# Kernel optimization log

Hardware: AMD Instinct MI355X
Metric: run time of the kernel (lower is better)

The kernel has to match this reference:

```python
import jax, jax.numpy as jnp
import numpy as np
from jax import lax

T, IMG, C_IN = 2048, 84, 4
HID = 256
NUM_OUT = 18
FEAT = 6 * 6 * 32  # 84 -> 42 -> 21 -> 11 -> 6 with stride-2 SAME convs


def setup_inputs() -> dict:
    key = jax.random.key(0)
    ks = jax.random.split(key, 8)
    d = {}
    d["x"] = jax.random.normal(ks[0], (T, IMG, IMG, C_IN), jnp.float32)
    cin = C_IN
    for i in range(4):
        d[f"conv_w{i}"] = jax.random.normal(ks[1 + i], (3, 3, cin, 32), jnp.float32) * (1.0 / np.sqrt(9 * cin))
        d[f"conv_b{i}"] = jnp.zeros((32,), jnp.float32)
        cin = 32
    d["lstm_w"] = jax.random.normal(ks[5], (FEAT + HID, 4 * HID), jnp.float32) * (1.0 / np.sqrt(FEAT + HID))
    d["lstm_b"] = jnp.zeros((4 * HID,), jnp.float32)
    d["fc_w"] = jax.random.normal(ks[6], (HID, NUM_OUT), jnp.float32) * 0.01
    d["fc_b"] = jnp.zeros((NUM_OUT,), jnp.float32)
    d["c_in"] = jnp.zeros((1, HID), jnp.float32)
    d["h_in"] = jnp.zeros((1, HID), jnp.float32)
    return d


def _conv_stack(x, ws, bs):
    dn = ("NHWC", "HWIO", "NHWC")
    for w, b in zip(ws, bs):
        x = jax.nn.elu(lax.conv_general_dilated(x, w, (2, 2), "SAME", dimension_numbers=dn) + b)
    return x.reshape(x.shape[0], -1)  # [T, FEAT]


def _lstm(feats, c0, h0, lstm_w, lstm_b):
    # BasicLSTMCell: gates [i, j, f, o], forget_bias = 1.0
    def step(carry, xt):
        c, h = carry  # [1, HID] each
        z = jnp.concatenate([xt[None, :], h], axis=1) @ lstm_w + lstm_b
        i, j, f, o = jnp.split(z, 4, axis=1)
        c = c * jax.nn.sigmoid(f + 1.0) + jax.nn.sigmoid(i) * jnp.tanh(j)
        h = jnp.tanh(c) * jax.nn.sigmoid(o)
        return (c, h), h[0]

    (_, _), hs = lax.scan(step, (c0, h0), feats)
    return hs  # [T, HID]


def reference(x, c_in, h_in,
              conv_w0, conv_b0, conv_w1, conv_b1,
              conv_w2, conv_b2, conv_w3, conv_b3,
              lstm_w, lstm_b, fc_w, fc_b):
    feats = _conv_stack(x, [conv_w0, conv_w1, conv_w2, conv_w3],
                        [conv_b0, conv_b1, conv_b2, conv_b3])
    hs = _lstm(feats, c_in, h_in, lstm_w, lstm_b)
    logits = hs @ fc_w + fc_b  # [T, NUM_OUT]
    return logits, hs
```

## Files before the change

kernel.cpp:

```cpp
#include <hip/hip_runtime.h>
#include <hip/hip_bf16.h>

__device__ inline float fsig(float x) { return 1.0f / (1.0f + __expf(-x)); }
__device__ inline float ftanh(float x) {
    float ax = fabsf(x);
    float e = __expf(-2.0f * ax);
    float r = (1.0f - e) / (1.0f + e);
    return x >= 0.0f ? r : -r;
}
__device__ inline float felu(float x) { return x > 0.0f ? x : expm1f(x); }

typedef _Float16 h2_t __attribute__((ext_vector_type(2)));

__device__ inline unsigned int packh2(float a, float b) {
    unsigned short ua = __builtin_bit_cast(unsigned short, (_Float16)a);
    unsigned short ub = __builtin_bit_cast(unsigned short, (_Float16)b);
    return (unsigned int)ua | ((unsigned int)ub << 16);
}
__device__ inline unsigned short f16bits(float a) {
    return __builtin_bit_cast(unsigned short, (_Float16)a);
}

__device__ inline float dot2acc(unsigned int w, unsigned int h, float acc) {
#if __has_builtin(__builtin_amdgcn_fdot2)
    return __builtin_amdgcn_fdot2(__builtin_bit_cast(h2_t, w), __builtin_bit_cast(h2_t, h), acc, false);
#else
    _Float16 wlo = __builtin_bit_cast(_Float16, (unsigned short)(w & 0xffff));
    _Float16 whi = __builtin_bit_cast(_Float16, (unsigned short)(w >> 16));
    _Float16 hlo = __builtin_bit_cast(_Float16, (unsigned short)(h & 0xffff));
    _Float16 hhi = __builtin_bit_cast(_Float16, (unsigned short)(h >> 16));
    return acc + (float)wlo * (float)hlo + (float)whi * (float)hhi;
#endif
}

__global__ __launch_bounds__(256) void conv0_kernel(const float* __restrict__ in,
                                                    const float* __restrict__ wg,
                                                    const float* __restrict__ bias,
                                                    unsigned short* __restrict__ out) {
    constexpr int W = 84, OW = 42, PAD = 0, WP = W + 2;
    __shared__ float in_s[3 * WP * 4];
    constexpr int NQ = 3 * WP;
    const int tid = threadIdx.x;
    const int oy = blockIdx.x;
    const int t = blockIdx.y;
    const int co = tid & 31;

    for (int q = tid; q < NQ; q += 256) {
        int ky = q / WP;
        int col = q - ky * WP;
        int iy = 2 * oy - PAD + ky;
        int ix = col - 1;
        float4 v = make_float4(0.f, 0.f, 0.f, 0.f);
        if (iy >= 0 && iy < W && ix >= 0 && ix < W)
            v = *(const float4*)&in[(((size_t)t * W + iy) * W + ix) * 4];
        *(float4*)&in_s[q * 4] = v;
    }

    float wr[9][4];
#pragma unroll
    for (int tap = 0; tap < 9; ++tap)
#pragma unroll
        for (int j = 0; j < 4; ++j) wr[tap][j] = wg[(tap * 4 + j) * 32 + co];
    __syncthreads();

    const int g = tid >> 5;
    constexpr int NOX = (OW + 7) / 8;
    float acc[NOX];
#pragma unroll
    for (int m = 0; m < NOX; ++m) acc[m] = 0.f;
#pragma unroll
    for (int ky = 0; ky < 3; ++ky)
#pragma unroll
        for (int kx = 0; kx < 3; ++kx) {
            float w0 = wr[ky * 3 + kx][0], w1 = wr[ky * 3 + kx][1];
            float w2 = wr[ky * 3 + kx][2], w3 = wr[ky * 3 + kx][3];
#pragma unroll
            for (int m = 0; m < NOX; ++m) {
                int ox = g + 8 * m;
                if (ox < OW) {
                    int cs = 2 * ox + kx - PAD + 1;
                    float4 xi = *(const float4*)&in_s[(ky * WP + cs) * 4];
                    acc[m] += xi.x * w0 + xi.y * w1 + xi.z * w2 + xi.w * w3;
                }
            }
        }
    float b = bias[co];
#pragma unroll
    for (int m = 0; m < NOX; ++m) {
        int ox = g + 8 * m;
        if (ox < OW)
            out[(((size_t)t * OW + oy) * OW + ox) * 32 + co] = f16bits(felu(acc[m] + b));
    }
}

template <int W, int OW, int PAD, bool F32OUT>
__global__ __launch_bounds__(256) void convh_kernel(const unsigned short* __restrict__ in,
                                                    const float* __restrict__ wg,
                                                    const float* __restrict__ bias,
                                                    void* __restrict__ outv) {
    constexpr int WP = W + 2;
    constexpr int OWH = (OW + 1) / 2;
    __shared__ __align__(16) unsigned short in_s[3][WP][32];
    __shared__ float zs[4][OW * 32];

    const int tid = threadIdx.x;
    const int oy = blockIdx.x;
    const int t = blockIdx.y;
    const int co = tid & 31;
    const int cig = (tid >> 5) & 3;
    const int oxh = tid >> 7;

    constexpr int NQ4 = 3 * WP * 4;
    uint4* in_s4 = reinterpret_cast<uint4*>(&in_s[0][0][0]);
    for (int q = tid; q < NQ4; q += 256) {
        int ky = q / (WP * 4);
        int rem = q - ky * (WP * 4);
        int col = rem >> 2, c4 = rem & 3;
        int iy = 2 * oy - PAD + ky;
        int ix = col - 1;
        uint4 v = make_uint4(0u, 0u, 0u, 0u);
        if (iy >= 0 && iy < W && ix >= 0 && ix < W)
            v = *(const uint4*)&in[(((size_t)t * W + iy) * W + ix) * 32 + c4 * 8];
        in_s4[q] = v;
    }

    unsigned int wr[9][4];
#pragma unroll
    for (int tap = 0; tap < 9; ++tap)
#pragma unroll
        for (int p = 0; p < 4; ++p)
            wr[tap][p] = packh2(wg[(tap * 32 + cig * 8 + 2 * p) * 32 + co],
                                wg[(tap * 32 + cig * 8 + 2 * p + 1) * 32 + co]);
    __syncthreads();

    float acc[OWH];
#pragma unroll
    for (int m = 0; m < OWH; ++m) acc[m] = 0.f;
#pragma unroll
    for (int ky = 0; ky < 3; ++ky)
#pragma unroll
        for (int kx = 0; kx < 3; ++kx) {
            unsigned int w0 = wr[ky * 3 + kx][0], w1 = wr[ky * 3 + kx][1];
            unsigned int w2 = wr[ky * 3 + kx][2], w3 = wr[ky * 3 + kx][3];
#pragma unroll
            for (int m = 0; m < OWH; ++m) {
                int ox = oxh * OWH + m;
                if (ox < OW) {
                    int cs = 2 * ox + kx - PAD + 1;
                    uint4 h8 = *(const uint4*)&in_s[ky][cs][cig * 8];
                    acc[m] = dot2acc(w0, h8.x, acc[m]);
                    acc[m] = dot2acc(w1, h8.y, acc[m]);
                    acc[m] = dot2acc(w2, h8.z, acc[m]);
                    acc[m] = dot2acc(w3, h8.w, acc[m]);
                }
            }
        }
#pragma unroll
    for (int m = 0; m < OWH; ++m) {
        int ox = oxh * OWH + m;
        if (ox < OW) zs[cig][ox * 32 + co] = acc[m];
    }
    __syncthreads();

    for (int idx = tid; idx < OW * 32; idx += 256) {
        float s = zs[0][idx] + zs[1][idx] + zs[2][idx] + zs[3][idx] + bias[idx & 31];
        s = felu(s);
        if constexpr (F32OUT)
            ((float*)outv)[(((size_t)t * OW + oy) * OW) * 32 + idx] = s;
        else
            ((unsigned short*)outv)[(((size_t)t * OW + oy) * OW) * 32 + idx] = f16bits(s);
    }
}

__global__ void gemm_kernel(const float* __restrict__ A, const float* __restrict__ Wx,
                            const float* __restrict__ bias, float* __restrict__ C) {
    __shared__ float As[32][64];
    __shared__ float Bs[32][64];
    const int bn = blockIdx.x, bm = blockIdx.y;
    const int tx = threadIdx.x, ty = threadIdx.y;
    const int tid = ty * 16 + tx;
    float acc[4][4] = {};
    for (int k0 = 0; k0 < 1152; k0 += 32) {
        {
            int r = tid >> 3;
            int c = (tid & 7) * 4;
            float4 a0 = *(const float4*)&A[(size_t)(bm * 64 + r) * 1152 + k0 + c];
            float4 a1 = *(const float4*)&A[(size_t)(bm * 64 + r + 32) * 1152 + k0 + c];
            As[c + 0][r] = a0.x; As[c + 1][r] = a0.y; As[c + 2][r] = a0.z; As[c + 3][r] = a0.w;
            As[c + 0][r + 32] = a1.x; As[c + 1][r + 32] = a1.y; As[c + 2][r + 32] = a1.z; As[c + 3][r + 32] = a1.w;
            int rb = tid >> 4;
            int cb = (tid & 15) * 4;
            *(float4*)&Bs[rb][cb] = *(const float4*)&Wx[(size_t)(k0 + rb) * 1024 + bn * 64 + cb];
            *(float4*)&Bs[rb + 16][cb] = *(const float4*)&Wx[(size_t)(k0 + rb + 16) * 1024 + bn * 64 + cb];
        }
        __syncthreads();
#pragma unroll
        for (int kk = 0; kk < 32; ++kk) {
            float4 a = *(float4*)&As[kk][ty * 4];
            float4 b = *(float4*)&Bs[kk][tx * 4];
            acc[0][0] += a.x * b.x; acc[0][1] += a.x * b.y; acc[0][2] += a.x * b.z; acc[0][3] += a.x * b.w;
            acc[1][0] += a.y * b.x; acc[1][1] += a.y * b.y; acc[1][2] += a.y * b.z; acc[1][3] += a.y * b.w;
            acc[2][0] += a.z * b.x; acc[2][1] += a.z * b.y; acc[2][2] += a.z * b.z; acc[2][3] += a.z * b.w;
            acc[3][0] += a.w * b.x; acc[3][1] += a.w * b.y; acc[3][2] += a.w * b.z; acc[3][3] += a.w * b.w;
        }
        __syncthreads();
    }
#pragma unroll
    for (int i = 0; i < 4; ++i) {
        int row = bm * 64 + ty * 4 + i;
#pragma unroll
        for (int j = 0; j < 4; ++j) {
            int col = bn * 64 + tx * 4 + j;
            C[(size_t)row * 1024 + col] = acc[i][j] + bias[col];
        }
    }
}

__global__ __launch_bounds__(512) void lstm9_kernel(const float* __restrict__ lstm_w,
                                                    const float* __restrict__ xpart,
                                                    const float* __restrict__ c_in,
                                                    const float* __restrict__ h_in,
                                                    float* __restrict__ hs_out) {
    __shared__ __align__(16) unsigned int wl[512][52];
    __shared__ __align__(16) unsigned short hpk[2][256];

    const int tid = threadIdx.x;
    const int wv = tid >> 6;
    const int l = tid & 63;
    const int s = l >> 5;
    const int u0 = (wv << 5) + (l & 31);

    for (int q = 0; q < 4; ++q)
        for (int p = 0; p < 12; ++p)
            wl[tid][q * 12 + p] = packh2(
                lstm_w[(size_t)(1152 + 128 * s + 2 * p) * 1024 + (q << 8) + u0],
                lstm_w[(size_t)(1152 + 128 * s + 2 * p + 1) * 1024 + (q << 8) + u0]);
    unsigned int wreg[4][52];
#pragma unroll
    for (int q = 0; q < 4; ++q)
        for (int p = 12; p < 64; ++p)
            wreg[q][p - 12] = packh2(
                lstm_w[(size_t)(1152 + 128 * s + 2 * p) * 1024 + (q << 8) + u0],
                lstm_w[(size_t)(1152 + 128 * s + 2 * p + 1) * 1024 + (q << 8) + u0]);

    float c_state = c_in[u0];
    if (tid < 256) hpk[0][tid] = f16bits(h_in[tid]);
    __syncthreads();

    float xp0 = xpart[u0], xp1 = xpart[256 + u0], xp2 = xpart[512 + u0], xp3 = xpart[768 + u0];

    for (int t = 0; t < 2048; ++t) {
        const int cur = t & 1;
        const uint4* hq = reinterpret_cast<const uint4*>(&hpk[cur][s << 7]);

        float a0 = 0.f, a1 = 0.f, a2 = 0.f, a3 = 0.f;
        {
            uint4 hA = hq[0], hB = hq[1], hC = hq[2];
            uint4 w0a = *(const uint4*)&wl[tid][0];
            uint4 w0b = *(const uint4*)&wl[tid][4];
            uint4 w0c = *(const uint4*)&wl[tid][8];
            a0 = dot2acc(w0a.x, hA.x, a0); a0 = dot2acc(w0a.y, hA.y, a0);
            a0 = dot2acc(w0a.z, hA.z, a0); a0 = dot2acc(w0a.w, hA.w, a0);
            a0 = dot2acc(w0b.x, hB.x, a0); a0 = dot2acc(w0b.y, hB.y, a0);
            a0 = dot2acc(w0b.z, hB.z, a0); a0 = dot2acc(w0b.w, hB.w, a0);
            a0 = dot2acc(w0c.x, hC.x, a0); a0 = dot2acc(w0c.y, hC.y, a0);
            a0 = dot2acc(w0c.z, hC.z, a0); a0 = dot2acc(w0c.w, hC.w, a0);
            uint4 w1a = *(const uint4*)&wl[tid][12];
            uint4 w1b = *(const uint4*)&wl[tid][16];
            uint4 w1c = *(const uint4*)&wl[tid][20];
            a1 = dot2acc(w1a.x, hA.x, a1); a1 = dot2acc(w1a.y, hA.y, a1);
            a1 = dot2acc(w1a.z, hA.z, a1); a1 = dot2acc(w1a.w, hA.w, a1);
            a1 = dot2acc(w1b.x, hB.x, a1); a1 = dot2acc(w1b.y, hB.y, a1);
            a1 = dot2acc(w1b.z, hB.z, a1); a1 = dot2acc(w1b.w, hB.w, a1);
            a1 = dot2acc(w1c.x, hC.x, a1); a1 = dot2acc(w1c.y, hC.y, a1);
            a1 = dot2acc(w1c.z, hC.z, a1); a1 = dot2acc(w1c.w, hC.w, a1);
            uint4 w2a = *(const uint4*)&wl[tid][24];
            uint4 w2b = *(const uint4*)&wl[tid][28];
            uint4 w2c = *(const uint4*)&wl[tid][32];
            a2 = dot2acc(w2a.x, hA.x, a2); a2 = dot2acc(w2a.y, hA.y, a2);
            a2 = dot2acc(w2a.z, hA.z, a2); a2 = dot2acc(w2a.w, hA.w, a2);
            a2 = dot2acc(w2b.x, hB.x, a2); a2 = dot2acc(w2b.y, hB.y, a2);
            a2 = dot2acc(w2b.z, hB.z, a2); a2 = dot2acc(w2b.w, hB.w, a2);
            a2 = dot2acc(w2c.x, hC.x, a2); a2 = dot2acc(w2c.y, hC.y, a2);
            a2 = dot2acc(w2c.z, hC.z, a2); a2 = dot2acc(w2c.w, hC.w, a2);
            uint4 w3a = *(const uint4*)&wl[tid][36];
            uint4 w3b = *(const uint4*)&wl[tid][40];
            uint4 w3c = *(const uint4*)&wl[tid][44];
            a3 = dot2acc(w3a.x, hA.x, a3); a3 = dot2acc(w3a.y, hA.y, a3);
            a3 = dot2acc(w3a.z, hA.z, a3); a3 = dot2acc(w3a.w, hA.w, a3);
            a3 = dot2acc(w3b.x, hB.x, a3); a3 = dot2acc(w3b.y, hB.y, a3);
            a3 = dot2acc(w3b.z, hB.z, a3); a3 = dot2acc(w3b.w, hB.w, a3);
            a3 = dot2acc(w3c.x, hC.x, a3); a3 = dot2acc(w3c.y, hC.y, a3);
            a3 = dot2acc(w3c.z, hC.z, a3); a3 = dot2acc(w3c.w, hC.w, a3);
        }
#pragma unroll
        for (int c = 3; c < 16; ++c) {
            uint4 h4 = hq[c];
            const int r = 4 * (c - 3);
            a0 = dot2acc(wreg[0][r + 0], h4.x, a0); a0 = dot2acc(wreg[0][r + 1], h4.y, a0);
            a0 = dot2acc(wreg[0][r + 2], h4.z, a0); a0 = dot2acc(wreg[0][r + 3], h4.w, a0);
            a1 = dot2acc(wreg[1][r + 0], h4.x, a1); a1 = dot2acc(wreg[1][r + 1], h4.y, a1);
            a1 = dot2acc(wreg[1][r + 2], h4.z, a1); a1 = dot2acc(wreg[1][r + 3], h4.w, a1);
            a2 = dot2acc(wreg[2][r + 0], h4.x, a2); a2 = dot2acc(wreg[2][r + 1], h4.y, a2);
            a2 = dot2acc(wreg[2][r + 2], h4.z, a2); a2 = dot2acc(wreg[2][r + 3], h4.w, a2);
            a3 = dot2acc(wreg[3][r + 0], h4.x, a3); a3 = dot2acc(wreg[3][r + 1], h4.y, a3);
            a3 = dot2acc(wreg[3][r + 2], h4.z, a3); a3 = dot2acc(wreg[3][r + 3], h4.w, a3);
        }

        float xn0 = 0.f, xn1 = 0.f, xn2 = 0.f, xn3 = 0.f;
        if (t + 1 < 2048) {
            const float* xr = &xpart[(size_t)(t + 1) * 1024];
            xn0 = xr[u0]; xn1 = xr[256 + u0]; xn2 = xr[512 + u0]; xn3 = xr[768 + u0];
        }

        float zi = a0 + __shfl_xor(a0, 32, 64) + xp0;
        float zj = a1 + __shfl_xor(a1, 32, 64) + xp1;
        float zf = a2 + __shfl_xor(a2, 32, 64) + xp2;
        float zo = a3 + __shfl_xor(a3, 32, 64) + xp3;

        c_state = c_state * fsig(zf + 1.0f) + fsig(zi) * ftanh(zj);
        float h = ftanh(c_state) * fsig(zo);
        if (s == 0) {
            hs_out[(size_t)t * 256 + u0] = h;
            hpk[cur ^ 1][u0] = f16bits(h);
        }

        asm volatile("s_waitcnt lgkmcnt(0)\n\ts_barrier" ::: "memory");
        xp0 = xn0; xp1 = xn1; xp2 = xn2; xp3 = xn3;
    }
}

__global__ void logits_kernel(const float* __restrict__ hs, const float* __restrict__ fc_w,
                              const float* __restrict__ fc_b, float* __restrict__ out) {
    int idx = blockIdx.x * 256 + threadIdx.x;
    if (idx >= 2048 * 18) return;
    int t = idx / 18, n = idx % 18;
    float acc = fc_b[n];
    const float* hrow = hs + (size_t)t * 256;
#pragma unroll 4
    for (int k = 0; k < 256; ++k) acc += hrow[k] * fc_w[k * 18 + n];
    out[idx] = acc;
}

extern "C" void kernel_launch(void* const* d_in, const int* in_sizes, int n_in,
                              void* d_out, int out_size, void* d_ws, size_t ws_size,
                              hipStream_t stream) {
    const float* x   = (const float*)d_in[0];
    const float* w0  = (const float*)d_in[1];
    const float* b0  = (const float*)d_in[2];
    const float* w1  = (const float*)d_in[3];
    const float* b1  = (const float*)d_in[4];
    const float* w2  = (const float*)d_in[5];
    const float* b2  = (const float*)d_in[6];
    const float* w3  = (const float*)d_in[7];
    const float* b3  = (const float*)d_in[8];
    const float* lw  = (const float*)d_in[9];
    const float* lb  = (const float*)d_in[10];
    const float* fcw = (const float*)d_in[11];
    const float* fcb = (const float*)d_in[12];
    const float* cin = (const float*)d_in[13];
    const float* hin = (const float*)d_in[14];

    float* outp = (float*)d_out;
    float* hs_out = outp + 2048 * 18;

    const size_t FIXED_B = ((size_t)2048 * 1152 + (size_t)2048 * 1024) * 4;
    const size_t PERT_B = ((size_t)56448 + 14112 + 3872) * 2;

    int C = 128;
    const int cands[5] = {2048, 1024, 512, 256, 128};
    for (int i = 0; i < 5; ++i) {
        if (FIXED_B + (size_t)cands[i] * PERT_B <= ws_size) { C = cands[i]; break; }
    }

    float* feats = (float*)d_ws;
    float* xpart = feats + (size_t)2048 * 1152;
    unsigned short* c0buf = (unsigned short*)(xpart + (size_t)2048 * 1024);
    unsigned short* c1buf = c0buf + (size_t)C * 56448;
    unsigned short* c2buf = c1buf + (size_t)C * 14112;

    for (int t0 = 0; t0 < 2048; t0 += C) {
        const float* xin = x + (size_t)t0 * 84 * 84 * 4;
        conv0_kernel<<<dim3(42, C), 256, 0, stream>>>(xin, w0, b0, c0buf);
        convh_kernel<42, 21, 0, false><<<dim3(21, C), 256, 0, stream>>>(c0buf, w1, b1, c1buf);
        convh_kernel<21, 11, 1, false><<<dim3(11, C), 256, 0, stream>>>(c1buf, w2, b2, c2buf);
        convh_kernel<11, 6, 1, true><<<dim3(6, C), 256, 0, stream>>>(c2buf, w3, b3,
                                                                     feats + (size_t)t0 * 1152);
    }

    gemm_kernel<<<dim3(16, 32), dim3(16, 16), 0, stream>>>(feats, lw, lb, xpart);
    lstm9_kernel<<<1, 512, 0, stream>>>(lw, xpart, cin, hin, hs_out);
    logits_kernel<<<144, 256, 0, stream>>>(hs_out, fcw, fcb, outp);
}
```

Baseline: 4.337 ms.

## Fuse conv stack, GEMM and LSTM into one persistent kernel with overlapped chunks

All conv layers, the input-projection GEMM and the LSTM recurrence now run in one persistent launch of 256 blocks. Block 0 runs the sequential LSTM and waits on per-chunk counters. The other 255 blocks work through 128-timestep chunks of conv layers and GEMM, separated by global atomic barriers. This lets the LSTM scan start on early chunks while later chunks are still being convolved, hiding the conv front end behind the serial recurrence. The cost is spin-wait barriers, which need every block to be resident at once (deadlock risk otherwise), a fixed chunk size, and a different LSTM reduction layout.

```diff
diff --git a/kernel.cpp b/kernel.cpp
--- a/kernel.cpp
+++ b/kernel.cpp
@@ -1,5 +1,8 @@
 #include <hip/hip_runtime.h>
 #include <hip/hip_bf16.h>
+
+#define AGENT __HIP_MEMORY_SCOPE_AGENT
+#define NW 255
 
 __device__ inline float fsig(float x) { return 1.0f / (1.0f + __expf(-x)); }
 __device__ inline float ftanh(float x) {
@@ -33,29 +36,47 @@
 #endif
 }
 
-__global__ __launch_bounds__(256) void conv0_kernel(const float* __restrict__ in,
-                                                    const float* __restrict__ wg,
-                                                    const float* __restrict__ bias,
-                                                    unsigned short* __restrict__ out) {
-    constexpr int W = 84, OW = 42, PAD = 0, WP = W + 2;
-    __shared__ float in_s[3 * WP * 4];
-    constexpr int NQ = 3 * WP;
+__global__ void init_kernel(unsigned int* ctrs) {
+    int i = threadIdx.x;
+    if (i < 80) ctrs[i] = 0u;
+}
+
+__device__ inline void layer_barrier(unsigned int* ctr) {
+    __syncthreads();
+    if (threadIdx.x == 0) {
+        __threadfence();
+        __hip_atomic_fetch_add(ctr, 1u, __ATOMIC_RELEASE, AGENT);
+        while (__hip_atomic_load(ctr, __ATOMIC_ACQUIRE, AGENT) < (unsigned)NW)
+            __builtin_amdgcn_s_sleep(2);
+    }
+    __syncthreads();
+}
+
+__device__ inline void lstm_wait_chunk(unsigned int* ctrs, int c) {
+    if (threadIdx.x == 0) {
+        unsigned int* f = ctrs + c * 5 + 4;
+        while (__hip_atomic_load(f, __ATOMIC_ACQUIRE, AGENT) < (unsigned)NW)
+            __builtin_amdgcn_s_sleep(2);
+    }
+    __syncthreads();
+}
+
+__device__ void conv0_item(const float* __restrict__ x, const float* __restrict__ wg,
+                           const float* __restrict__ bias, unsigned short* __restrict__ out,
+                           int tg, int tl, int oy, unsigned char* smraw) {
+    constexpr int W = 84, OW = 42, WP = 86;
+    float* in_s = (float*)smraw;
     const int tid = threadIdx.x;
-    const int oy = blockIdx.x;
-    const int t = blockIdx.y;
     const int co = tid & 31;
 
-    for (int q = tid; q < NQ; q += 256) {
-        int ky = q / WP;
-        int col = q - ky * WP;
-        int iy = 2 * oy - PAD + ky;
-        int ix = col - 1;
+    for (int q = tid; q < 3 * WP; q += 512) {
+        int ky = q / WP, col = q - ky * WP;
+        int iy = 2 * oy + ky, ix = col - 1;
         float4 v = make_float4(0.f, 0.f, 0.f, 0.f);
-        if (iy >= 0 && iy < W && ix >= 0 && ix < W)
-            v = *(const float4*)&in[(((size_t)t * W + iy) * W + ix) * 4];
+        if (iy < W && ix >= 0 && ix < W)
+            v = *(const float4*)&x[(((size_t)tg * W + iy) * W + ix) * 4];
         *(float4*)&in_s[q * 4] = v;
     }
-
     float wr[9][4];
 #pragma unroll
     for (int tap = 0; tap < 9; ++tap)
@@ -64,10 +85,7 @@
     __syncthreads();
 
     const int g = tid >> 5;
-    constexpr int NOX = (OW + 7) / 8;
-    float acc[NOX];
-#pragma unroll
-    for (int m = 0; m < NOX; ++m) acc[m] = 0.f;
+    float acc[3] = {0.f, 0.f, 0.f};
 #pragma unroll
     for (int ky = 0; ky < 3; ++ky)
 #pragma unroll
@@ -75,10 +93,10 @@
             float w0 = wr[ky * 3 + kx][0], w1 = wr[ky * 3 + kx][1];
             float w2 = wr[ky * 3 + kx][2], w3 = wr[ky * 3 + kx][3];
 #pragma unroll
-            for (int m = 0; m < NOX; ++m) {
-                int ox = g + 8 * m;
+            for (int m = 0; m < 3; ++m) {
+                int ox = g + 16 * m;
                 if (ox < OW) {
-                    int cs = 2 * ox + kx - PAD + 1;
+                    int cs = 2 * ox + kx + 1;
                     float4 xi = *(const float4*)&in_s[(ky * WP + cs) * 4];
                     acc[m] += xi.x * w0 + xi.y * w1 + xi.z * w2 + xi.w * w3;
                 }
@@ -86,44 +104,39 @@
         }
     float b = bias[co];
 #pragma unroll
-    for (int m = 0; m < NOX; ++m) {
-        int ox = g + 8 * m;
+    for (int m = 0; m < 3; ++m) {
+        int ox = g + 16 * m;
         if (ox < OW)
-            out[(((size_t)t * OW + oy) * OW + ox) * 32 + co] = f16bits(felu(acc[m] + b));
-    }
+            out[(((size_t)tl * OW + oy) * OW + ox) * 32 + co] = f16bits(felu(acc[m] + b));
+    }
+    __syncthreads();
 }
 
 template <int W, int OW, int PAD, bool F32OUT>
-__global__ __launch_bounds__(256) void convh_kernel(const unsigned short* __restrict__ in,
-                                                    const float* __restrict__ wg,
-                                                    const float* __restrict__ bias,
-                                                    void* __restrict__ outv) {
+__device__ void convh_item(const unsigned short* __restrict__ in, const float* __restrict__ wg,
+                           const float* __restrict__ bias, void* __restrict__ outv,
+                           int tl_in, int oy, size_t orow, unsigned char* smraw) {
     constexpr int WP = W + 2;
-    constexpr int OWH = (OW + 1) / 2;
-    __shared__ __align__(16) unsigned short in_s[3][WP][32];
-    __shared__ float zs[4][OW * 32];
-
+    constexpr int OWQ = (OW + 3) / 4;
+    unsigned short* in_s = (unsigned short*)smraw;
+    float* zs = (float*)(smraw + 8448);
     const int tid = threadIdx.x;
-    const int oy = blockIdx.x;
-    const int t = blockIdx.y;
     const int co = tid & 31;
     const int cig = (tid >> 5) & 3;
-    const int oxh = tid >> 7;
-
-    constexpr int NQ4 = 3 * WP * 4;
-    uint4* in_s4 = reinterpret_cast<uint4*>(&in_s[0][0][0]);
-    for (int q = tid; q < NQ4; q += 256) {
+    const int oxq = tid >> 7;
+
+    const int NQ4 = 3 * WP * 4;
+    uint4* in_s4 = (uint4*)in_s;
+    for (int q = tid; q < NQ4; q += 512) {
         int ky = q / (WP * 4);
-        int rem = q - ky * (WP * 4);
+        int rem = q - ky * WP * 4;
         int col = rem >> 2, c4 = rem & 3;
-        int iy = 2 * oy - PAD + ky;
-        int ix = col - 1;
+        int iy = 2 * oy - PAD + ky, ix = col - 1;
         uint4 v = make_uint4(0u, 0u, 0u, 0u);
         if (iy >= 0 && iy < W && ix >= 0 && ix < W)
-            v = *(const uint4*)&in[(((size_t)t * W + iy) * W + ix) * 32 + c4 * 8];
+            v = *(const uint4*)&in[(((size_t)tl_in * W + iy) * W + ix) * 32 + c4 * 8];
         in_s4[q] = v;
     }
-
     unsigned int wr[9][4];
 #pragma unroll
     for (int tap = 0; tap < 9; ++tap)
@@ -133,9 +146,9 @@
                                 wg[(tap * 32 + cig * 8 + 2 * p + 1) * 32 + co]);
     __syncthreads();
 
-    float acc[OWH];
-#pragma unroll
-    for (int m = 0; m < OWH; ++m) acc[m] = 0.f;
+    float acc[OWQ];
+#pragma unroll
+    for (int m = 0; m < OWQ; ++m) acc[m] = 0.f;
 #pragma unroll
     for (int ky = 0; ky < 3; ++ky)
 #pragma unroll
@@ -143,11 +156,11 @@
             unsigned int w0 = wr[ky * 3 + kx][0], w1 = wr[ky * 3 + kx][1];
             unsigned int w2 = wr[ky * 3 + kx][2], w3 = wr[ky * 3 + kx][3];
 #pragma unroll
-            for (int m = 0; m < OWH; ++m) {
-                int ox = oxh * OWH + m;
+            for (int m = 0; m < OWQ; ++m) {
+                int ox = oxq * OWQ + m;
                 if (ox < OW) {
                     int cs = 2 * ox + kx - PAD + 1;
-                    uint4 h8 = *(const uint4*)&in_s[ky][cs][cig * 8];
+                    uint4 h8 = *(const uint4*)&in_s[(ky * WP + cs) * 32 + cig * 8];
                     acc[m] = dot2acc(w0, h8.x, acc[m]);
                     acc[m] = dot2acc(w1, h8.y, acc[m]);
                     acc[m] = dot2acc(w2, h8.z, acc[m]);
@@ -156,177 +169,234 @@
             }
         }
 #pragma unroll
-    for (int m = 0; m < OWH; ++m) {
-        int ox = oxh * OWH + m;
-        if (ox < OW) zs[cig][ox * 32 + co] = acc[m];
-    }
-    __syncthreads();
-
-    for (int idx = tid; idx < OW * 32; idx += 256) {
-        float s = zs[0][idx] + zs[1][idx] + zs[2][idx] + zs[3][idx] + bias[idx & 31];
+    for (int m = 0; m < OWQ; ++m) {
+        int ox = oxq * OWQ + m;
+        if (ox < OW) zs[cig * OW * 32 + ox * 32 + co] = acc[m];
+    }
+    __syncthreads();
+
+    for (int idx = tid; idx < OW * 32; idx += 512) {
+        float s = zs[idx] + zs[OW * 32 + idx] + zs[2 * OW * 32 + idx] + zs[3 * OW * 32 + idx] +
+                  bias[idx & 31];
         s = felu(s);
         if constexpr (F32OUT)
-            ((float*)outv)[(((size_t)t * OW + oy) * OW) * 32 + idx] = s;
+            ((float*)outv)[((orow * OW + oy) * OW) * 32 + idx] = s;
         else
-            ((unsigned short*)outv)[(((size_t)t * OW + oy) * OW) * 32 + idx] = f16bits(s);
-    }
-}
-
-__global__ void gemm_kernel(const float* __restrict__ A, const float* __restrict__ Wx,
-                            const float* __restrict__ bias, float* __restrict__ C) {
-    __shared__ float As[32][64];
-    __shared__ float Bs[32][64];
-    const int bn = blockIdx.x, bm = blockIdx.y;
-    const int tx = threadIdx.x, ty = threadIdx.y;
-    const int tid = ty * 16 + tx;
+            ((unsigned short*)outv)[((orow * OW + oy) * OW) * 32 + idx] = f16bits(s);
+    }
+    __syncthreads();
+}
+
+__device__ void gemm_item(const float* __restrict__ A, const float* __restrict__ Wx,
+                          const float* __restrict__ bias, float* __restrict__ C,
+                          int bm, int bn, unsigned char* smraw) {
+    float* As = (float*)smraw;
+    float* Bs = (float*)(smraw + 8192);
+    const int tid = threadIdx.x;
+    const bool act = tid < 256;
+    const int tx = tid & 15, ty = (tid >> 4) & 15;
     float acc[4][4] = {};
     for (int k0 = 0; k0 < 1152; k0 += 32) {
-        {
+        if (act) {
             int r = tid >> 3;
             int c = (tid & 7) * 4;
             float4 a0 = *(const float4*)&A[(size_t)(bm * 64 + r) * 1152 + k0 + c];
             float4 a1 = *(const float4*)&A[(size_t)(bm * 64 + r + 32) * 1152 + k0 + c];
-            As[c + 0][r] = a0.x; As[c + 1][r] = a0.y; As[c + 2][r] = a0.z; As[c + 3][r] = a0.w;
-            As[c + 0][r + 32] = a1.x; As[c + 1][r + 32] = a1.y; As[c + 2][r + 32] = a1.z; As[c + 3][r + 32] = a1.w;
+            As[(c + 0) * 64 + r] = a0.x; As[(c + 1) * 64 + r] = a0.y;
+            As[(c + 2) * 64 + r] = a0.z; As[(c + 3) * 64 + r] = a0.w;
+            As[(c + 0) * 64 + r + 32] = a1.x; As[(c + 1) * 64 + r + 32] = a1.y;
+            As[(c + 2) * 64 + r + 32] = a1.z; As[(c + 3) * 64 + r + 32] = a1.w;
             int rb = tid >> 4;
             int cb = (tid & 15) * 4;
-            *(float4*)&Bs[rb][cb] = *(const float4*)&Wx[(size_t)(k0 + rb) * 1024 + bn * 64 + cb];
-            *(float4*)&Bs[rb + 16][cb] = *(const float4*)&Wx[(size_t)(k0 + rb + 16) * 1024 + bn * 64 + cb];
+            *(float4*)&Bs[rb * 64 + cb] = *(const float4*)&Wx[(size_t)(k0 + rb) * 1024 + bn * 64 + cb];
+            *(float4*)&Bs[(rb + 16) * 64 + cb] =
+                *(const float4*)&Wx[(size_t)(k0 + rb + 16) * 1024 + bn * 64 + cb];
         }
         __syncthreads();
-#pragma unroll
-        for (int kk = 0; kk < 32; ++kk) {
-            float4 a = *(float4*)&As[kk][ty * 4];
-            float4 b = *(float4*)&Bs[kk][tx * 4];
-            acc[0][0] += a.x * b.x; acc[0][1] += a.x * b.y; acc[0][2] += a.x * b.z; acc[0][3] += a.x * b.w;
-            acc[1][0] += a.y * b.x; acc[1][1] += a.y * b.y; acc[1][2] += a.y * b.z; acc[1][3] += a.y * b.w;
-            acc[2][0] += a.z * b.x; acc[2][1] += a.z * b.y; acc[2][2] += a.z * b.z; acc[2][3] += a.z * b.w;
-            acc[3][0] += a.w * b.x; acc[3][1] += a.w * b.y; acc[3][2] += a.w * b.z; acc[3][3] += a.w * b.w;
+        if (act) {
+#pragma unroll
+            for (int kk = 0; kk < 32; ++kk) {
+                float4 a = *(float4*)&As[kk * 64 + ty * 4];
+                float4 b = *(float4*)&Bs[kk * 64 + tx * 4];
+                acc[0][0] += a.x * b.x; acc[0][1] += a.x * b.y; acc[0][2] += a.x * b.z; acc[0][3] += a.x * b.w;
+                acc[1][0] += a.y * b.x; acc[1][1] += a.y * b.y; acc[1][2] += a.y * b.z; acc[1][3] += a.y * b.w;
+                acc[2][0] += a.z * b.x; acc[2][1] += a.z * b.y; acc[2][2] += a.z * b.z; acc[2][3] += a.z * b.w;
+                acc[3][0] += a.w * b.x; acc[3][1] += a.w * b.y; acc[3][2] += a.w * b.z; acc[3][3] += a.w * b.w;
+            }
         }
         __syncthreads();
     }
-#pragma unroll
-    for (int i = 0; i < 4; ++i) {
-        int row = bm * 64 + ty * 4 + i;
-#pragma unroll
-        for (int j = 0; j < 4; ++j) {
-            int col = bn * 64 + tx * 4 + j;
-            C[(size_t)row * 1024 + col] = acc[i][j] + bias[col];
-        }
-    }
-}
-
-__global__ __launch_bounds__(512) void lstm9_kernel(const float* __restrict__ lstm_w,
-                                                    const float* __restrict__ xpart,
-                                                    const float* __restrict__ c_in,
-                                                    const float* __restrict__ h_in,
-                                                    float* __restrict__ hs_out) {
-    __shared__ __align__(16) unsigned int wl[512][52];
-    __shared__ __align__(16) unsigned short hpk[2][256];
-
+    if (act) {
+#pragma unroll
+        for (int i = 0; i < 4; ++i) {
+            int row = bm * 64 + ty * 4 + i;
+#pragma unroll
+            for (int j = 0; j < 4; ++j) {
+                int col = bn * 64 + tx * 4 + j;
+                C[(size_t)row * 1024 + col] = acc[i][j] + bias[col];
+            }
+        }
+    }
+    __syncthreads();
+}
+
+__global__ __launch_bounds__(512) void mega_kernel(
+    const float* __restrict__ x, const float* __restrict__ w0, const float* __restrict__ b0,
+    const float* __restrict__ w1, const float* __restrict__ b1,
+    const float* __restrict__ w2, const float* __restrict__ b2,
+    const float* __restrict__ w3, const float* __restrict__ b3,
+    const float* __restrict__ lw, const float* __restrict__ lb,
+    const float* __restrict__ cin, const float* __restrict__ hin,
+    unsigned short* c0buf, unsigned short* c1buf, unsigned short* c2buf,
+    float* feats, float* xpart, unsigned int* ctrs, float* hs_out) {
+    __shared__ __align__(16) unsigned char smraw[115776];
+    const int bid = blockIdx.x;
     const int tid = threadIdx.x;
-    const int wv = tid >> 6;
-    const int l = tid & 63;
-    const int s = l >> 5;
-    const int u0 = (wv << 5) + (l & 31);
-
-    for (int q = 0; q < 4; ++q)
-        for (int p = 0; p < 12; ++p)
-            wl[tid][q * 12 + p] = packh2(
-                lstm_w[(size_t)(1152 + 128 * s + 2 * p) * 1024 + (q << 8) + u0],
-                lstm_w[(size_t)(1152 + 128 * s + 2 * p + 1) * 1024 + (q << 8) + u0]);
-    unsigned int wreg[4][52];
-#pragma unroll
-    for (int q = 0; q < 4; ++q)
-        for (int p = 12; p < 64; ++p)
-            wreg[q][p - 12] = packh2(
-                lstm_w[(size_t)(1152 + 128 * s + 2 * p) * 1024 + (q << 8) + u0],
-                lstm_w[(size_t)(1152 + 128 * s + 2 * p + 1) * 1024 + (q << 8) + u0]);
-
-    float c_state = c_in[u0];
-    if (tid < 256) hpk[0][tid] = f16bits(h_in[tid]);
-    __syncthreads();
-
-    float xp0 = xpart[u0], xp1 = xpart[256 + u0], xp2 = xpart[512 + u0], xp3 = xpart[768 + u0];
-
-    for (int t = 0; t < 2048; ++t) {
-        const int cur = t & 1;
-        const uint4* hq = reinterpret_cast<const uint4*>(&hpk[cur][s << 7]);
-
-        float a0 = 0.f, a1 = 0.f, a2 = 0.f, a3 = 0.f;
-        {
-            uint4 hA = hq[0], hB = hq[1], hC = hq[2];
-            uint4 w0a = *(const uint4*)&wl[tid][0];
-            uint4 w0b = *(const uint4*)&wl[tid][4];
-            uint4 w0c = *(const uint4*)&wl[tid][8];
-            a0 = dot2acc(w0a.x, hA.x, a0); a0 = dot2acc(w0a.y, hA.y, a0);
-            a0 = dot2acc(w0a.z, hA.z, a0); a0 = dot2acc(w0a.w, hA.w, a0);
-            a0 = dot2acc(w0b.x, hB.x, a0); a0 = dot2acc(w0b.y, hB.y, a0);
-            a0 = dot2acc(w0b.z, hB.z, a0); a0 = dot2acc(w0b.w, hB.w, a0);
-            a0 = dot2acc(w0c.x, hC.x, a0); a0 = dot2acc(w0c.y, hC.y, a0);
-            a0 = dot2acc(w0c.z, hC.z, a0); a0 = dot2acc(w0c.w, hC.w, a0);
-            uint4 w1a = *(const uint4*)&wl[tid][12];
-            uint4 w1b = *(const uint4*)&wl[tid][16];
-            uint4 w1c = *(const uint4*)&wl[tid][20];
-            a1 = dot2acc(w1a.x, hA.x, a1); a1 = dot2acc(w1a.y, hA.y, a1);
-            a1 = dot2acc(w1a.z, hA.z, a1); a1 = dot2acc(w1a.w, hA.w, a1);
-            a1 = dot2acc(w1b.x, hB.x, a1); a1 = dot2acc(w1b.y, hB.y, a1);
-            a1 = dot2acc(w1b.z, hB.z, a1); a1 = dot2acc(w1b.w, hB.w, a1);
-            a1 = dot2acc(w1c.x, hC.x, a1); a1 = dot2acc(w1c.y, hC.y, a1);
-            a1 = dot2acc(w1c.z, hC.z, a1); a1 = dot2acc(w1c.w, hC.w, a1);
-            uint4 w2a = *(const uint4*)&wl[tid][24];
-            uint4 w2b = *(const uint4*)&wl[tid][28];
-            uint4 w2c = *(const uint4*)&wl[tid][32];
-            a2 = dot2acc(w2a.x, hA.x, a2); a2 = dot2acc(w2a.y, hA.y, a2);
-            a2 = dot2acc(w2a.z, hA.z, a2); a2 = dot2acc(w2a.w, hA.w, a2);
-            a2 = dot2acc(w2b.x, hB.x, a2); a2 = dot2acc(w2b.y, hB.y, a2);
-            a2 = dot2acc(w2b.z, hB.z, a2); a2 = dot2acc(w2b.w, hB.w, a2);
-            a2 = dot2acc(w2c.x, hC.x, a2); a2 = dot2acc(w2c.y, hC.y, a2);
-            a2 = dot2acc(w2c.z, hC.z, a2); a2 = dot2acc(w2c.w, hC.w, a2);
-            uint4 w3a = *(const uint4*)&wl[tid][36];
-            uint4 w3b = *(const uint4*)&wl[tid][40];
-            uint4 w3c = *(const uint4*)&wl[tid][44];
-            a3 = dot2acc(w3a.x, hA.x, a3); a3 = dot2acc(w3a.y, hA.y, a3);
-            a3 = dot2acc(w3a.z, hA.z, a3); a3 = dot2acc(w3a.w, hA.w, a3);
-            a3 = dot2acc(w3b.x, hB.x, a3); a3 = dot2acc(w3b.y, hB.y, a3);
-            a3 = dot2acc(w3b.z, hB.z, a3); a3 = dot2acc(w3b.w, hB.w, a3);
-            a3 = dot2acc(w3c.x, hC.x, a3); a3 = dot2acc(w3c.y, hC.y, a3);
-            a3 = dot2acc(w3c.z, hC.z, a3); a3 = dot2acc(w3c.w, hC.w, a3);
-        }
-#pragma unroll
-        for (int c = 3; c < 16; ++c) {
-            uint4 h4 = hq[c];
-            const int r = 4 * (c - 3);
-            a0 = dot2acc(wreg[0][r + 0], h4.x, a0); a0 = dot2acc(wreg[0][r + 1], h4.y, a0);
-            a0 = dot2acc(wreg[0][r + 2], h4.z, a0); a0 = dot2acc(wreg[0][r + 3], h4.w, a0);
-            a1 = dot2acc(wreg[1][r + 0], h4.x, a1); a1 = dot2acc(wreg[1][r + 1], h4.y, a1);
-            a1 = dot2acc(wreg[1][r + 2], h4.z, a1); a1 = dot2acc(wreg[1][r + 3], h4.w, a1);
-            a2 = dot2acc(wreg[2][r + 0], h4.x, a2); a2 = dot2acc(wreg[2][r + 1], h4.y, a2);
-            a2 = dot2acc(wreg[2][r + 2], h4.z, a2); a2 = dot2acc(wreg[2][r + 3], h4.w, a2);
-            a3 = dot2acc(wreg[3][r + 0], h4.x, a3); a3 = dot2acc(wreg[3][r + 1], h4.y, a3);
-            a3 = dot2acc(wreg[3][r + 2], h4.z, a3); a3 = dot2acc(wreg[3][r + 3], h4.w, a3);
-        }
-
-        float xn0 = 0.f, xn1 = 0.f, xn2 = 0.f, xn3 = 0.f;
-        if (t + 1 < 2048) {
-            const float* xr = &xpart[(size_t)(t + 1) * 1024];
-            xn0 = xr[u0]; xn1 = xr[256 + u0]; xn2 = xr[512 + u0]; xn3 = xr[768 + u0];
-        }
-
-        float zi = a0 + __shfl_xor(a0, 32, 64) + xp0;
-        float zj = a1 + __shfl_xor(a1, 32, 64) + xp1;
-        float zf = a2 + __shfl_xor(a2, 32, 64) + xp2;
-        float zo = a3 + __shfl_xor(a3, 32, 64) + xp3;
-
-        c_state = c_state * fsig(zf + 1.0f) + fsig(zi) * ftanh(zj);
-        float h = ftanh(c_state) * fsig(zo);
-        if (s == 0) {
-            hs_out[(size_t)t * 256 + u0] = h;
-            hpk[cur ^ 1][u0] = f16bits(h);
-        }
-
-        asm volatile("s_waitcnt lgkmcnt(0)\n\ts_barrier" ::: "memory");
-        xp0 = xn0; xp1 = xn1; xp2 = xn2; xp3 = xn3;
+
+    if (bid == 0) {
+        unsigned int (*wl)[52] = reinterpret_cast<unsigned int(*)[52]>(smraw);
+        float (*zsm)[4][256] = reinterpret_cast<float(*)[4][256]>(smraw + 106496);
+        unsigned int (*hpk)[2][68] = reinterpret_cast<unsigned int(*)[2][68]>(smraw + 114688);
+
+        const int s = tid >> 8;
+        const int u = tid & 255;
+
+        for (int q = 0; q < 4; ++q)
+            for (int p = 0; p < 12; ++p) {
+                int gp = 64 * s + p;
+                wl[tid][q * 12 + p] = packh2(
+                    lw[(size_t)(1152 + 2 * gp) * 1024 + (q << 8) + u],
+                    lw[(size_t)(1152 + 2 * gp + 1) * 1024 + (q << 8) + u]);
+            }
+        unsigned int wreg[4][52];
+#pragma unroll
+        for (int q = 0; q < 4; ++q)
+            for (int p = 12; p < 64; ++p) {
+                int gp = 64 * s + p;
+                wreg[q][p - 12] = packh2(
+                    lw[(size_t)(1152 + 2 * gp) * 1024 + (q << 8) + u],
+                    lw[(size_t)(1152 + 2 * gp + 1) * 1024 + (q << 8) + u]);
+            }
+
+        float c_state = cin[u];
+        if (tid < 256) {
+            unsigned short* hrow = (unsigned short*)&hpk[0][u >> 7][0];
+            hrow[u & 127] = f16bits(hin[u]);
+        }
+        __syncthreads();
+
+        lstm_wait_chunk(ctrs, 0);
+        float xp0 = xpart[u], xp1 = xpart[256 + u], xp2 = xpart[512 + u], xp3 = xpart[768 + u];
+
+        for (int t = 0; t < 2048; ++t) {
+            const int cur = t & 1;
+            const uint4* hq = reinterpret_cast<const uint4*>(&hpk[cur][s][0]);
+
+            float a0 = 0.f, a1 = 0.f, a2 = 0.f, a3 = 0.f;
+            {
+                uint4 hA = hq[0], hB = hq[1], hC = hq[2];
+                uint4 w0a = *(const uint4*)&wl[tid][0];
+                uint4 w0b = *(const uint4*)&wl[tid][4];
+                uint4 w0c = *(const uint4*)&wl[tid][8];
+                a0 = dot2acc(w0a.x, hA.x, a0); a0 = dot2acc(w0a.y, hA.y, a0);
+                a0 = dot2acc(w0a.z, hA.z, a0); a0 = dot2acc(w0a.w, hA.w, a0);
+                a0 = dot2acc(w0b.x, hB.x, a0); a0 = dot2acc(w0b.y, hB.y, a0);
+                a0 = dot2acc(w0b.z, hB.z, a0); a0 = dot2acc(w0b.w, hB.w, a0);
+                a0 = dot2acc(w0c.x, hC.x, a0); a0 = dot2acc(w0c.y, hC.y, a0);
+                a0 = dot2acc(w0c.z, hC.z, a0); a0 = dot2acc(w0c.w, hC.w, a0);
+                uint4 w1a = *(const uint4*)&wl[tid][12];
+                uint4 w1b = *(const uint4*)&wl[tid][16];
+                uint4 w1c = *(const uint4*)&wl[tid][20];
+                a1 = dot2acc(w1a.x, hA.x, a1); a1 = dot2acc(w1a.y, hA.y, a1);
+                a1 = dot2acc(w1a.z, hA.z, a1); a1 = dot2acc(w1a.w, hA.w, a1);
+                a1 = dot2acc(w1b.x, hB.x, a1); a1 = dot2acc(w1b.y, hB.y, a1);
+                a1 = dot2acc(w1b.z, hB.z, a1); a1 = dot2acc(w1b.w, hB.w, a1);
+                a1 = dot2acc(w1c.x, hC.x, a1); a1 = dot2acc(w1c.y, hC.y, a1);
+                a1 = dot2acc(w1c.z, hC.z, a1); a1 = dot2acc(w1c.w, hC.w, a1);
+                uint4 w2a = *(const uint4*)&wl[tid][24];
+                uint4 w2b = *(const uint4*)&wl[tid][28];
+                uint4 w2c = *(const uint4*)&wl[tid][32];
+                a2 = dot2acc(w2a.x, hA.x, a2); a2 = dot2acc(w2a.y, hA.y, a2);
+                a2 = dot2acc(w2a.z, hA.z, a2); a2 = dot2acc(w2a.w, hA.w, a2);
+                a2 = dot2acc(w2b.x, hB.x, a2); a2 = dot2acc(w2b.y, hB.y, a2);
+                a2 = dot2acc(w2b.z, hB.z, a2); a2 = dot2acc(w2b.w, hB.w, a2);
+                a2 = dot2acc(w2c.x, hC.x, a2); a2 = dot2acc(w2c.y, hC.y, a2);
+                a2 = dot2acc(w2c.z, hC.z, a2); a2 = dot2acc(w2c.w, hC.w, a2);
+                uint4 w3a = *(const uint4*)&wl[tid][36];
+                uint4 w3b = *(const uint4*)&wl[tid][40];
+                uint4 w3c = *(const uint4*)&wl[tid][44];
+                a3 = dot2acc(w3a.x, hA.x, a3); a3 = dot2acc(w3a.y, hA.y, a3);
+                a3 = dot2acc(w3a.z, hA.z, a3); a3 = dot2acc(w3a.w, hA.w, a3);
+                a3 = dot2acc(w3b.x, hB.x, a3); a3 = dot2acc(w3b.y, hB.y, a3);
+                a3 = dot2acc(w3b.z, hB.z, a3); a3 = dot2acc(w3b.w, hB.w, a3);
+                a3 = dot2acc(w3c.x, hC.x, a3); a3 = dot2acc(w3c.y, hC.y, a3);
+                a3 = dot2acc(w3c.z, hC.z, a3); a3 = dot2acc(w3c.w, hC.w, a3);
+            }
+#pragma unroll
+            for (int c = 3; c < 16; ++c) {
+                uint4 h4 = hq[c];
+                const int r = 4 * (c - 3);
+                a0 = dot2acc(wreg[0][r + 0], h4.x, a0); a0 = dot2acc(wreg[0][r + 1], h4.y, a0);
+                a0 = dot2acc(wreg[0][r + 2], h4.z, a0); a0 = dot2acc(wreg[0][r + 3], h4.w, a0);
+                a1 = dot2acc(wreg[1][r + 0], h4.x, a1); a1 = dot2acc(wreg[1][r + 1], h4.y, a1);
+                a1 = dot2acc(wreg[1][r + 2], h4.z, a1); a1 = dot2acc(wreg[1][r + 3], h4.w, a1);
+                a2 = dot2acc(wreg[2][r + 0], h4.x, a2); a2 = dot2acc(wreg[2][r + 1], h4.y, a2);
+                a2 = dot2acc(wreg[2][r + 2], h4.z, a2); a2 = dot2acc(wreg[2][r + 3], h4.w, a2);
+                a3 = dot2acc(wreg[3][r + 0], h4.x, a3); a3 = dot2acc(wreg[3][r + 1], h4.y, a3);
+                a3 = dot2acc(wreg[3][r + 2], h4.z, a3); a3 = dot2acc(wreg[3][r + 3], h4.w, a3);
+            }
+            zsm[s][0][u] = a0;
+            zsm[s][1][u] = a1;
+            zsm[s][2][u] = a2;
+            zsm[s][3][u] = a3;
+
+            float xn0 = 0.f, xn1 = 0.f, xn2 = 0.f, xn3 = 0.f;
+            if (t + 1 < 2048) {
+                if (((t + 1) & 127) == 0) lstm_wait_chunk(ctrs, (t + 1) >> 7);
+                const float* xr = &xpart[(size_t)(t + 1) * 1024];
+                xn0 = xr[u]; xn1 = xr[256 + u]; xn2 = xr[512 + u]; xn3 = xr[768 + u];
+            }
+
+            asm volatile("s_waitcnt lgkmcnt(0)\n\ts_barrier" ::: "memory");
+
+            float zi = zsm[0][0][u] + zsm[1][0][u] + xp0;
+            float zj = zsm[0][1][u] + zsm[1][1][u] + xp1;
+            float zf = zsm[0][2][u] + zsm[1][2][u] + xp2;
+            float zo = zsm[0][3][u] + zsm[1][3][u] + xp3;
+            c_state = c_state * fsig(zf + 1.0f) + fsig(zi) * ftanh(zj);
+            float h = ftanh(c_state) * fsig(zo);
+            if (tid < 256) {
+                hs_out[(size_t)t * 256 + u] = h;
+                unsigned short* hrow = (unsigned short*)&hpk[cur ^ 1][u >> 7][0];
+                hrow[u & 127] = f16bits(h);
+            }
+
+            asm volatile("s_waitcnt lgkmcnt(0)\n\ts_barrier" ::: "memory");
+            xp0 = xn0; xp1 = xn1; xp2 = xn2; xp3 = xn3;
+        }
+    } else {
+        const int wid = bid - 1;
+        for (int c = 0; c < 16; ++c) {
+            const int base = c * 128;
+            for (int i = wid; i < 42 * 128; i += NW)
+                conv0_item(x, w0, b0, c0buf, base + i / 42, i / 42, i % 42, smraw);
+            layer_barrier(&ctrs[c * 5 + 0]);
+            for (int i = wid; i < 21 * 128; i += NW)
+                convh_item<42, 21, 0, false>(c0buf, w1, b1, c1buf, i / 21, i % 21,
+                                             (size_t)(i / 21), smraw);
+            layer_barrier(&ctrs[c * 5 + 1]);
+            for (int i = wid; i < 11 * 128; i += NW)
+                convh_item<21, 11, 1, false>(c1buf, w2, b2, c2buf, i / 11, i % 11,
+                                             (size_t)(i / 11), smraw);
+            layer_barrier(&ctrs[c * 5 + 2]);
+            for (int i = wid; i < 6 * 128; i += NW)
+                convh_item<11, 6, 1, true>(c2buf, w3, b3, feats, i / 6, i % 6,
+                                           (size_t)(base + i / 6), smraw);
+            layer_barrier(&ctrs[c * 5 + 3]);
+            for (int i = wid; i < 32; i += NW)
+                gemm_item(feats, lw, lb, xpart, c * 2 + (i >> 4), i & 15, smraw);
+            layer_barrier(&ctrs[c * 5 + 4]);
+        }
     }
 }
 
@@ -364,31 +434,15 @@
     float* outp = (float*)d_out;
     float* hs_out = outp + 2048 * 18;
 
-    const size_t FIXED_B = ((size_t)2048 * 1152 + (size_t)2048 * 1024) * 4;
-    const size_t PERT_B = ((size_t)56448 + 14112 + 3872) * 2;
-
-    int C = 128;
-    const int cands[5] = {2048, 1024, 512, 256, 128};
-    for (int i = 0; i < 5; ++i) {
-        if (FIXED_B + (size_t)cands[i] * PERT_B <= ws_size) { C = cands[i]; break; }
-    }
-
     float* feats = (float*)d_ws;
     float* xpart = feats + (size_t)2048 * 1152;
     unsigned short* c0buf = (unsigned short*)(xpart + (size_t)2048 * 1024);
-    unsigned short* c1buf = c0buf + (size_t)C * 56448;
-    unsigned short* c2buf = c1buf + (size_t)C * 14112;
-
-    for (int t0 = 0; t0 < 2048; t0 += C) {
-        const float* xin = x + (size_t)t0 * 84 * 84 * 4;
-        conv0_kernel<<<dim3(42, C), 256, 0, stream>>>(xin, w0, b0, c0buf);
-        convh_kernel<42, 21, 0, false><<<dim3(21, C), 256, 0, stream>>>(c0buf, w1, b1, c1buf);
-        convh_kernel<21, 11, 1, false><<<dim3(11, C), 256, 0, stream>>>(c1buf, w2, b2, c2buf);
-        convh_kernel<11, 6, 1, true><<<dim3(6, C), 256, 0, stream>>>(c2buf, w3, b3,
-                                                                     feats + (size_t)t0 * 1152);
-    }
-
-    gemm_kernel<<<dim3(16, 32), dim3(16, 16), 0, stream>>>(feats, lw, lb, xpart);
-    lstm9_kernel<<<1, 512, 0, stream>>>(lw, xpart, cin, hin, hs_out);
+    unsigned short* c1buf = c0buf + (size_t)128 * 56448;
+    unsigned short* c2buf = c1buf + (size_t)128 * 14112;
+    unsigned int* ctrs = (unsigned int*)(c2buf + (size_t)128 * 3872);
+
+    init_kernel<<<1, 128, 0, stream>>>(ctrs);
+    mega_kernel<<<256, 512, 0, stream>>>(x, w0, b0, w1, b1, w2, b2, w3, b3, lw, lb, cin, hin,
+                                         c0buf, c1buf, c2buf, feats, xpart, ctrs, hs_out);
     logits_kernel<<<144, 256, 0, stream>>>(hs_out, fcw, fcb, outp);
 }
```

Result: slower. 7.718 ms (+78.0%).
